# Performance work log

Hardware: AMD Instinct MI355X
Metric: run time of the kernel (lower is better)

The kernel has to match this reference:

```python
import jax, jax.numpy as jnp
import numpy as np
import math

B, S_MAX, D = 16, 4096, 4096
H, H_KV, D_H = 32, 8, 128
REP = H // H_KV
START_POS = S_MAX - 1  # decode at last slot -> attend over full cache


def _rope(t, cos, sin):
    # t: [B, 1, h, D_H]; cos/sin: [1, D_H//2] (per-position rotary factors)
    b, s, h, dh = t.shape
    tr = t.reshape(b, s, h, dh // 2, 2)
    e, o = tr[..., 0], tr[..., 1]          # even / odd components
    c = cos[None, :, None, :]              # [1, 1, 1, D_H//2]
    sn = sin[None, :, None, :]
    out = jnp.stack([e * c - o * sn, e * sn + o * c], axis=-1)
    return out.reshape(b, s, h, dh)


def setup_inputs() -> dict:
    key = jax.random.key(0)
    ks = jax.random.split(key, 8)
    x = jax.random.normal(ks[0], (B, 1, D), dtype=jnp.float32)
    cache_k = jax.random.normal(ks[1], (B, S_MAX, H_KV, D_H), dtype=jnp.float32) * 0.02
    cache_v = jax.random.normal(ks[2], (B, S_MAX, H_KV, D_H), dtype=jnp.float32) * 0.02
    wq = jax.random.normal(ks[3], (D, H * D_H), dtype=jnp.float32) * 0.02
    wk = jax.random.normal(ks[4], (D, H_KV * D_H), dtype=jnp.float32) * 0.02
    wv = jax.random.normal(ks[5], (D, H_KV * D_H), dtype=jnp.float32) * 0.02
    wo = jax.random.normal(ks[6], (H * D_H, D), dtype=jnp.float32) * 0.02
    # real RoPE angles for position START_POS
    inv_freq = 1.0 / (10000.0 ** (np.arange(0, D_H, 2, dtype=np.float32) / D_H))
    ang = np.float32(START_POS) * inv_freq  # [D_H//2]
    freqs_cos = jnp.asarray(np.cos(ang))[None, :]  # [1, 64]
    freqs_sin = jnp.asarray(np.sin(ang))[None, :]
    return {"x": x, "cache_k": cache_k, "cache_v": cache_v,
            "wq": wq, "wk": wk, "wv": wv, "wo": wo,
            "freqs_cos": freqs_cos, "freqs_sin": freqs_sin,
            "start_pos": START_POS}


def reference(x, cache_k, cache_v, wq, wk, wv, wo, freqs_cos, freqs_sin, start_pos):
    b = x.shape[0]
    xq = (x @ wq).reshape(b, 1, H, D_H)
    xk = (x @ wk).reshape(b, 1, H_KV, D_H)
    xv = (x @ wv).reshape(b, 1, H_KV, D_H)
    xq = _rope(xq, freqs_cos, freqs_sin)
    xk = _rope(xk, freqs_cos, freqs_sin)
    # KV-cache append (start_pos is a Python int -> static slice)
    cache_k = jax.lax.dynamic_update_slice(cache_k, xk, (0, start_pos, 0, 0))
    cache_v = jax.lax.dynamic_update_slice(cache_v, xv, (0, start_pos, 0, 0))
    L = start_pos + 1
    keys = cache_k[:, :L]    # [B, L, H_KV, D_H]
    # NOTE: original has `values = repeat_kv(keys, num_rep)` -- values == keys (bug),
    # reproduced faithfully here. cache_v is still written, matching the original.
    q = xq.reshape(b, 1, H_KV, REP, D_H)
    # GQA scores without materializing the repeated KV tensor
    scores = jnp.einsum('bqkrd,bskd->bkrqs', q, keys) / math.sqrt(D_H)
    attn = jax.nn.softmax(scores, axis=-1)
    out = jnp.einsum('bkrqs,bskd->bqkrd', attn, keys)  # values == keys (faithful bug)
    out = out.reshape(b, 1, H * D_H) @ wo
    return out
```

## Files before the change

kernel.cpp:

```cpp
#include <hip/hip_runtime.h>
#include <math.h>

#define BATCH 16
#define SMAX 4096
#define DMODEL 4096
#define NH 32
#define NKV 8
#define NREP 4
#define DH 128
#define QKCOLS 5120
#define NCHUNK 8
#define CHUNK 512
#define TILE 64

__global__ __launch_bounds__(256) void gemv_part(
    const float* __restrict__ in,
    const float* __restrict__ w1, int c1,
    const float* __restrict__ w2, int c2,
    float* __restrict__ part)
{
    const int tile = blockIdx.x;
    const int ch = blockIdx.y;
    const int t = threadIdx.x;
    const int col = tile * 256 + t;
    const int totC = c1 + c2;
    const int d0 = ch * 256;

    __shared__ float xs[BATCH * 256];
    for (int b = 0; b < BATCH; ++b)
        xs[b * 256 + t] = in[(size_t)b * DMODEL + d0 + t];
    __syncthreads();

    const float* w; int stride, wcol;
    if (col < c1) { w = w1; stride = c1; wcol = col; }
    else          { w = w2; stride = c2; wcol = col - c1; }

    float acc[BATCH];
#pragma unroll
    for (int b = 0; b < BATCH; ++b) acc[b] = 0.f;

    const float* wp = w + (size_t)d0 * stride + wcol;
    for (int d = 0; d < 256; d += 4) {
        float wa = wp[(size_t)(d + 0) * stride];
        float wb = wp[(size_t)(d + 1) * stride];
        float wc = wp[(size_t)(d + 2) * stride];
        float wd = wp[(size_t)(d + 3) * stride];
#pragma unroll
        for (int b = 0; b < BATCH; ++b) {
            const float4 xv = *(const float4*)&xs[b * 256 + d];
            float a = acc[b];
            a = fmaf(xv.x, wa, a);
            a = fmaf(xv.y, wb, a);
            a = fmaf(xv.z, wc, a);
            a = fmaf(xv.w, wd, a);
            acc[b] = a;
        }
    }
#pragma unroll
    for (int b = 0; b < BATCH; ++b)
        part[((size_t)ch * BATCH + b) * totC + col] = acc[b];
}

__global__ __launch_bounds__(256) void rope_reduce(
    const float* __restrict__ part,
    const float* __restrict__ fcos, const float* __restrict__ fsin,
    float* __restrict__ xqk)
{
    int g = blockIdx.x * 256 + threadIdx.x;
    int b = g / 2560;
    int po = g % 2560;
    float e = 0.f, o = 0.f;
    const float* p = part + (size_t)b * QKCOLS + 2 * po;
#pragma unroll
    for (int ch = 0; ch < 16; ++ch) {
        float2 v = *(const float2*)(p + (size_t)ch * BATCH * QKCOLS);
        e += v.x; o += v.y;
    }
    int i = po & 63;
    float c = fcos[i], s = fsin[i];
    xqk[(size_t)b * QKCOLS + 2 * po]     = e * c - o * s;
    xqk[(size_t)b * QKCOLS + 2 * po + 1] = e * s + o * c;
}

__global__ __launch_bounds__(256) void attn_part_kernel(
    const float* __restrict__ cache_k,
    const float* __restrict__ xqk,
    const int* __restrict__ sp,
    float* __restrict__ out)
{
    const int chunk = blockIdx.x;
    const int kv = blockIdx.y;
    const int b = blockIdx.z;
    const int t = threadIdx.x;
    const int dl = t & 63;
    const int r = t >> 6;
    const int start_pos = sp[0];

    __shared__ float k_lds[TILE * DH];

    const int h = kv * NREP + r;
    const float* qp = xqk + (size_t)b * QKCOLS + h * DH;
    const int half = dl & 31;
    const int hi = dl >> 5;
    float4 q4 = *(const float4*)(qp + half * 4);
    const float scale = 0.08838834764831845f;
    q4.x *= scale; q4.y *= scale; q4.z *= scale; q4.w *= scale;
    const int row_owned = (half << 1) + hi;

    const float* xknew = xqk + (size_t)b * QKCOLS + DMODEL + kv * DH;
    const float* kbase = cache_k + ((size_t)b * SMAX * NKV + kv) * DH;

    float m_run = -1e30f, l_run = 0.f;
    float2 acc = make_float2(0.f, 0.f);

    for (int tt = 0; tt < CHUNK / TILE; ++tt) {
        const int s_base = chunk * CHUNK + tt * TILE;
#pragma unroll
        for (int it = 0; it < 8; ++it) {
            int f = it * 256 + t;
            int row = f >> 5;
            int c4 = (f & 31) * 4;
            int s = s_base + row;
            const float* src = (s == start_pos) ? (xknew + c4)
                             : (kbase + (size_t)s * (NKV * DH) + c4);
            *(float4*)&k_lds[row * DH + c4] = *(const float4*)src;
        }
        __syncthreads();

        float score_mine = -1e30f;
        for (int jp = 0; jp < 32; ++jp) {
            int row = 2 * jp + hi;
            const float4 k4 = *(const float4*)&k_lds[row * DH + half * 4];
            float partial = q4.x * k4.x + q4.y * k4.y + q4.z * k4.z + q4.w * k4.w;
#pragma unroll
            for (int m = 1; m < 32; m <<= 1)
                partial += __shfl_xor(partial, m, 64);
            if (half == jp) score_mine = partial;
        }
        if (s_base + row_owned > start_pos) score_mine = -1e30f;

        float m_tile = score_mine;
#pragma unroll
        for (int m = 1; m < 64; m <<= 1)
            m_tile = fmaxf(m_tile, __shfl_xor(m_tile, m, 64));
        float m_new = fmaxf(m_run, m_tile);
        float alpha = __expf(m_run - m_new);
        float p_mine = __expf(score_mine - m_new);
        float psum = p_mine;
#pragma unroll
        for (int m = 1; m < 64; m <<= 1)
            psum += __shfl_xor(psum, m, 64);
        l_run = l_run * alpha + psum;
        acc.x *= alpha; acc.y *= alpha;
        m_run = m_new;

        for (int j = 0; j < 64; ++j) {
            int src_lane = (j >> 1) + ((j & 1) << 5);
            float pj = __shfl(p_mine, src_lane, 64);
            const float2 kj = *(const float2*)&k_lds[j * DH + 2 * dl];
            acc.x = fmaf(pj, kj.x, acc.x);
            acc.y = fmaf(pj, kj.y, acc.y);
        }
        __syncthreads();
    }

    float* rec = out + ((((size_t)b * NKV + kv) * NCHUNK + chunk) * NREP + r) * 130;
    rec[2 * dl] = acc.x;
    rec[2 * dl + 1] = acc.y;
    if (dl == 0) { rec[128] = m_run; rec[129] = l_run; }
}

__global__ __launch_bounds__(128) void attn_combine(
    const float* __restrict__ part, float* __restrict__ attn_out)
{
    const int hq = blockIdx.x;
    const int b = blockIdx.y;
    const int kv = hq >> 2, r = hq & 3;
    const int d = threadIdx.x;
    float m_c[NCHUNK], l_c[NCHUNK];
    float M = -1e30f;
#pragma unroll
    for (int c = 0; c < NCHUNK; ++c) {
        const float* rec = part + ((((size_t)b * NKV + kv) * NCHUNK + c) * NREP + r) * 130;
        m_c[c] = rec[128]; l_c[c] = rec[129];
        M = fmaxf(M, m_c[c]);
    }
    float num = 0.f, den = 0.f;
#pragma unroll
    for (int c = 0; c < NCHUNK; ++c) {
        const float* rec = part + ((((size_t)b * NKV + kv) * NCHUNK + c) * NREP + r) * 130;
        float w = __expf(m_c[c] - M);
        num = fmaf(w, rec[d], num);
        den = fmaf(w, l_c[c], den);
    }
    attn_out[(size_t)b * DMODEL + hq * DH + d] = num / den;
}

__global__ __launch_bounds__(256) void reduce_out(
    const float* __restrict__ part, float* __restrict__ out)
{
    int g = blockIdx.x * 256 + threadIdx.x;
    int b = g >> 12, o = g & 4095;
    float s = 0.f;
#pragma unroll
    for (int ch = 0; ch < 16; ++ch)
        s += part[((size_t)ch * BATCH + b) * DMODEL + o];
    out[g] = s;
}

extern "C" void kernel_launch(void* const* d_in, const int* in_sizes, int n_in,
                              void* d_out, int out_size, void* d_ws, size_t ws_size,
                              hipStream_t stream) {
    const float* x       = (const float*)d_in[0];
    const float* cache_k = (const float*)d_in[1];
    const float* wq      = (const float*)d_in[3];
    const float* wk      = (const float*)d_in[4];
    const float* wo      = (const float*)d_in[6];
    const float* fcos    = (const float*)d_in[7];
    const float* fsin    = (const float*)d_in[8];
    const int*   sp      = (const int*)d_in[9];
    float* out = (float*)d_out;
    float* ws  = (float*)d_ws;

    float* part_qk   = ws;
    float* xqk       = part_qk + 1310720;
    float* attn_part = xqk + 81920;
    float* attn_out  = attn_part + 532480;
    float* part_out  = part_qk;

    gemv_part<<<dim3(QKCOLS / 256, 16), 256, 0, stream>>>(x, wq, 4096, wk, 1024, part_qk);
    rope_reduce<<<160, 256, 0, stream>>>(part_qk, fcos, fsin, xqk);
    attn_part_kernel<<<dim3(NCHUNK, NKV, BATCH), 256, 0, stream>>>(cache_k, xqk, sp, attn_part);
    attn_combine<<<dim3(NH, BATCH), 128, 0, stream>>>(attn_part, attn_out);
    gemv_part<<<dim3(DMODEL / 256, 16), 256, 0, stream>>>(attn_out, wo, 4096, nullptr, 0, part_out);
    reduce_out<<<256, 256, 0, stream>>>(part_out, out);
}
```

Measured before the change: 734.7 us.

## Restructure attention to compute all GQA heads per tile and split GEMV depth finer

```diff
diff --git a/kernel.cpp b/kernel.cpp
--- a/kernel.cpp
+++ b/kernel.cpp
@@ -12,47 +12,52 @@
 #define NCHUNK 8
 #define CHUNK 512
 #define TILE 64
+#define NDCH 32
+#define DCH 128
+#define RECS 132
+
+__global__ __launch_bounds__(256) void transpose_x(
+    const float* __restrict__ x, float* __restrict__ xt)
+{
+    int g = blockIdx.x * 256 + threadIdx.x;
+    int b = g >> 12, d = g & 4095;
+    xt[d * BATCH + b] = x[g];
+}
 
 __global__ __launch_bounds__(256) void gemv_part(
-    const float* __restrict__ in,
+    const float* __restrict__ xt,
     const float* __restrict__ w1, int c1,
     const float* __restrict__ w2, int c2,
     float* __restrict__ part)
 {
-    const int tile = blockIdx.x;
+    const int col = blockIdx.x * 256 + threadIdx.x;
     const int ch = blockIdx.y;
-    const int t = threadIdx.x;
-    const int col = tile * 256 + t;
     const int totC = c1 + c2;
-    const int d0 = ch * 256;
-
-    __shared__ float xs[BATCH * 256];
-    for (int b = 0; b < BATCH; ++b)
-        xs[b * 256 + t] = in[(size_t)b * DMODEL + d0 + t];
-    __syncthreads();
+    const int d0 = ch * DCH;
 
     const float* w; int stride, wcol;
     if (col < c1) { w = w1; stride = c1; wcol = col; }
     else          { w = w2; stride = c2; wcol = col - c1; }
 
+    const float* wp = w + (size_t)d0 * stride + wcol;
+    const float* xp = xt + d0 * BATCH;
+
     float acc[BATCH];
 #pragma unroll
     for (int b = 0; b < BATCH; ++b) acc[b] = 0.f;
 
-    const float* wp = w + (size_t)d0 * stride + wcol;
-    for (int d = 0; d < 256; d += 4) {
+    for (int d = 0; d < DCH; d += 4) {
         float wa = wp[(size_t)(d + 0) * stride];
         float wb = wp[(size_t)(d + 1) * stride];
         float wc = wp[(size_t)(d + 2) * stride];
         float wd = wp[(size_t)(d + 3) * stride];
 #pragma unroll
         for (int b = 0; b < BATCH; ++b) {
-            const float4 xv = *(const float4*)&xs[b * 256 + d];
             float a = acc[b];
-            a = fmaf(xv.x, wa, a);
-            a = fmaf(xv.y, wb, a);
-            a = fmaf(xv.z, wc, a);
-            a = fmaf(xv.w, wd, a);
+            a = fmaf(xp[(d + 0) * BATCH + b], wa, a);
+            a = fmaf(xp[(d + 1) * BATCH + b], wb, a);
+            a = fmaf(xp[(d + 2) * BATCH + b], wc, a);
+            a = fmaf(xp[(d + 3) * BATCH + b], wd, a);
             acc[b] = a;
         }
     }
@@ -72,7 +77,7 @@
     float e = 0.f, o = 0.f;
     const float* p = part + (size_t)b * QKCOLS + 2 * po;
 #pragma unroll
-    for (int ch = 0; ch < 16; ++ch) {
+    for (int ch = 0; ch < NDCH; ++ch) {
         float2 v = *(const float2*)(p + (size_t)ch * BATCH * QKCOLS);
         e += v.x; o += v.y;
     }
@@ -86,92 +91,151 @@
     const float* __restrict__ cache_k,
     const float* __restrict__ xqk,
     const int* __restrict__ sp,
-    float* __restrict__ out)
+    float* __restrict__ outp)
 {
     const int chunk = blockIdx.x;
     const int kv = blockIdx.y;
     const int b = blockIdx.z;
     const int t = threadIdx.x;
-    const int dl = t & 63;
-    const int r = t >> 6;
+    const int lane = t & 63;
+    const int w = t >> 6;
     const int start_pos = sp[0];
 
-    __shared__ float k_lds[TILE * DH];
-
-    const int h = kv * NREP + r;
-    const float* qp = xqk + (size_t)b * QKCOLS + h * DH;
-    const int half = dl & 31;
-    const int hi = dl >> 5;
-    float4 q4 = *(const float4*)(qp + half * 4);
-    const float scale = 0.08838834764831845f;
-    q4.x *= scale; q4.y *= scale; q4.z *= scale; q4.w *= scale;
-    const int row_owned = (half << 1) + hi;
-
+    __shared__ __align__(16) float k_lds[TILE * DH];
+    __shared__ __align__(16) float p_lds[TILE * NREP];
+    __shared__ __align__(16) float alpha_lds[NREP];
+
+    const float* qw = xqk + (size_t)b * QKCOLS + (kv * NREP + w) * DH;
     const float* xknew = xqk + (size_t)b * QKCOLS + DMODEL + kv * DH;
     const float* kbase = cache_k + ((size_t)b * SMAX * NKV + kv) * DH;
-
+    const float scale = 0.08838834764831845f;
+
+    const int jhalf = lane >> 5, cqo = lane & 31;
     float m_run = -1e30f, l_run = 0.f;
-    float2 acc = make_float2(0.f, 0.f);
+    float4 acc[NREP];
+#pragma unroll
+    for (int r = 0; r < NREP; ++r) acc[r] = make_float4(0.f, 0.f, 0.f, 0.f);
+
+    float4 pf[8];
+    {
+        int s_base = chunk * CHUNK;
+#pragma unroll
+        for (int it = 0; it < 8; ++it) {
+            int f = it * 256 + t, row = f >> 5, cq = f & 31;
+            int s = s_base + row;
+            const float* src = (s == start_pos) ? (xknew + 4 * cq)
+                             : (kbase + (size_t)s * (NKV * DH) + 4 * cq);
+            pf[it] = *(const float4*)src;
+        }
+    }
 
     for (int tt = 0; tt < CHUNK / TILE; ++tt) {
         const int s_base = chunk * CHUNK + tt * TILE;
+        __syncthreads();
 #pragma unroll
         for (int it = 0; it < 8; ++it) {
-            int f = it * 256 + t;
-            int row = f >> 5;
-            int c4 = (f & 31) * 4;
-            int s = s_base + row;
-            const float* src = (s == start_pos) ? (xknew + c4)
-                             : (kbase + (size_t)s * (NKV * DH) + c4);
-            *(float4*)&k_lds[row * DH + c4] = *(const float4*)src;
+            int f = it * 256 + t, row = f >> 5, cq = f & 31;
+            *(float4*)&k_lds[row * DH + 4 * (cq ^ (row & 7))] = pf[it];
         }
         __syncthreads();
-
-        float score_mine = -1e30f;
-        for (int jp = 0; jp < 32; ++jp) {
-            int row = 2 * jp + hi;
-            const float4 k4 = *(const float4*)&k_lds[row * DH + half * 4];
-            float partial = q4.x * k4.x + q4.y * k4.y + q4.z * k4.z + q4.w * k4.w;
-#pragma unroll
-            for (int m = 1; m < 32; m <<= 1)
-                partial += __shfl_xor(partial, m, 64);
-            if (half == jp) score_mine = partial;
-        }
-        if (s_base + row_owned > start_pos) score_mine = -1e30f;
-
-        float m_tile = score_mine;
+        if (tt + 1 < CHUNK / TILE) {
+            int nb = s_base + TILE;
+#pragma unroll
+            for (int it = 0; it < 8; ++it) {
+                int f = it * 256 + t, row = f >> 5, cq = f & 31;
+                int s = nb + row;
+                const float* src = (s == start_pos) ? (xknew + 4 * cq)
+                                 : (kbase + (size_t)s * (NKV * DH) + 4 * cq);
+                pf[it] = *(const float4*)src;
+            }
+        }
+
+        float sc = 0.f;
+#pragma unroll
+        for (int cq = 0; cq < 32; ++cq) {
+            const float4 k4 = *(const float4*)&k_lds[lane * DH + 4 * (cq ^ (lane & 7))];
+            sc += qw[4 * cq + 0] * k4.x + qw[4 * cq + 1] * k4.y
+                + qw[4 * cq + 2] * k4.z + qw[4 * cq + 3] * k4.w;
+        }
+        sc *= scale;
+        const bool valid = (s_base + lane) <= start_pos;
+        sc = valid ? sc : -1e30f;
+
+        float m_tile = sc;
 #pragma unroll
         for (int m = 1; m < 64; m <<= 1)
             m_tile = fmaxf(m_tile, __shfl_xor(m_tile, m, 64));
         float m_new = fmaxf(m_run, m_tile);
         float alpha = __expf(m_run - m_new);
-        float p_mine = __expf(score_mine - m_new);
-        float psum = p_mine;
+        float p = valid ? __expf(sc - m_new) : 0.f;
+        float ps = p;
 #pragma unroll
         for (int m = 1; m < 64; m <<= 1)
-            psum += __shfl_xor(psum, m, 64);
-        l_run = l_run * alpha + psum;
-        acc.x *= alpha; acc.y *= alpha;
+            ps += __shfl_xor(ps, m, 64);
+        l_run = l_run * alpha + ps;
         m_run = m_new;
-
-        for (int j = 0; j < 64; ++j) {
-            int src_lane = (j >> 1) + ((j & 1) << 5);
-            float pj = __shfl(p_mine, src_lane, 64);
-            const float2 kj = *(const float2*)&k_lds[j * DH + 2 * dl];
-            acc.x = fmaf(pj, kj.x, acc.x);
-            acc.y = fmaf(pj, kj.y, acc.y);
-        }
+        p_lds[lane * NREP + w] = p;
+        if (lane == 0) alpha_lds[w] = alpha;
         __syncthreads();
-    }
-
-    float* rec = out + ((((size_t)b * NKV + kv) * NCHUNK + chunk) * NREP + r) * 130;
-    rec[2 * dl] = acc.x;
-    rec[2 * dl + 1] = acc.y;
-    if (dl == 0) { rec[128] = m_run; rec[129] = l_run; }
+
+        const float4 a4 = *(const float4*)alpha_lds;
+        float al[NREP] = { a4.x, a4.y, a4.z, a4.w };
+#pragma unroll
+        for (int r = 0; r < NREP; ++r) {
+            acc[r].x *= al[r]; acc[r].y *= al[r];
+            acc[r].z *= al[r]; acc[r].w *= al[r];
+        }
+#pragma unroll
+        for (int jj = 0; jj < 8; ++jj) {
+            const int j = 16 * w + 8 * jhalf + jj;
+            const float4 p4 = *(const float4*)&p_lds[j * NREP];
+            const float4 k4 = *(const float4*)&k_lds[j * DH + 4 * (cqo ^ jj)];
+            acc[0].x = fmaf(p4.x, k4.x, acc[0].x);
+            acc[0].y = fmaf(p4.x, k4.y, acc[0].y);
+            acc[0].z = fmaf(p4.x, k4.z, acc[0].z);
+            acc[0].w = fmaf(p4.x, k4.w, acc[0].w);
+            acc[1].x = fmaf(p4.y, k4.x, acc[1].x);
+            acc[1].y = fmaf(p4.y, k4.y, acc[1].y);
+            acc[1].z = fmaf(p4.y, k4.z, acc[1].z);
+            acc[1].w = fmaf(p4.y, k4.w, acc[1].w);
+            acc[2].x = fmaf(p4.z, k4.x, acc[2].x);
+            acc[2].y = fmaf(p4.z, k4.y, acc[2].y);
+            acc[2].z = fmaf(p4.z, k4.z, acc[2].z);
+            acc[2].w = fmaf(p4.z, k4.w, acc[2].w);
+            acc[3].x = fmaf(p4.w, k4.x, acc[3].x);
+            acc[3].y = fmaf(p4.w, k4.y, acc[3].y);
+            acc[3].z = fmaf(p4.w, k4.z, acc[3].z);
+            acc[3].w = fmaf(p4.w, k4.w, acc[3].w);
+        }
+    }
+
+    __syncthreads();
+    float* dst = &k_lds[t * 16];
+    *(float4*)(dst + 0)  = acc[0];
+    *(float4*)(dst + 4)  = acc[1];
+    *(float4*)(dst + 8)  = acc[2];
+    *(float4*)(dst + 12) = acc[3];
+    __syncthreads();
+    if (t < 128) {
+        const int cq2 = t & 31, rep = t >> 5;
+        float4 sum = make_float4(0.f, 0.f, 0.f, 0.f);
+#pragma unroll
+        for (int src = 0; src < 8; ++src) {
+            int tsrc = (src >> 1) * 64 + (src & 1) * 32 + cq2;
+            const float4 v = *(const float4*)&k_lds[tsrc * 16 + rep * 4];
+            sum.x += v.x; sum.y += v.y; sum.z += v.z; sum.w += v.w;
+        }
+        float* rec = outp + ((((size_t)b * NKV + kv) * NCHUNK + chunk) * NREP + rep) * RECS;
+        *(float4*)&rec[4 * cq2] = sum;
+    }
+    if (lane == 0) {
+        float* rec = outp + ((((size_t)b * NKV + kv) * NCHUNK + chunk) * NREP + w) * RECS;
+        rec[128] = m_run; rec[129] = l_run;
+    }
 }
 
 __global__ __launch_bounds__(128) void attn_combine(
-    const float* __restrict__ part, float* __restrict__ attn_out)
+    const float* __restrict__ part, float* __restrict__ attn_out_t)
 {
     const int hq = blockIdx.x;
     const int b = blockIdx.y;
@@ -181,19 +245,19 @@
     float M = -1e30f;
 #pragma unroll
     for (int c = 0; c < NCHUNK; ++c) {
-        const float* rec = part + ((((size_t)b * NKV + kv) * NCHUNK + c) * NREP + r) * 130;
+        const float* rec = part + ((((size_t)b * NKV + kv) * NCHUNK + c) * NREP + r) * RECS;
         m_c[c] = rec[128]; l_c[c] = rec[129];
         M = fmaxf(M, m_c[c]);
     }
     float num = 0.f, den = 0.f;
 #pragma unroll
     for (int c = 0; c < NCHUNK; ++c) {
-        const float* rec = part + ((((size_t)b * NKV + kv) * NCHUNK + c) * NREP + r) * 130;
-        float w = __expf(m_c[c] - M);
-        num = fmaf(w, rec[d], num);
-        den = fmaf(w, l_c[c], den);
-    }
-    attn_out[(size_t)b * DMODEL + hq * DH + d] = num / den;
+        const float* rec = part + ((((size_t)b * NKV + kv) * NCHUNK + c) * NREP + r) * RECS;
+        float wgt = __expf(m_c[c] - M);
+        num = fmaf(wgt, rec[d], num);
+        den = fmaf(wgt, l_c[c], den);
+    }
+    attn_out_t[(size_t)(hq * DH + d) * BATCH + b] = num / den;
 }
 
 __global__ __launch_bounds__(256) void reduce_out(
@@ -203,7 +267,7 @@
     int b = g >> 12, o = g & 4095;
     float s = 0.f;
 #pragma unroll
-    for (int ch = 0; ch < 16; ++ch)
+    for (int ch = 0; ch < NDCH; ++ch)
         s += part[((size_t)ch * BATCH + b) * DMODEL + o];
     out[g] = s;
 }
@@ -222,16 +286,18 @@
     float* out = (float*)d_out;
     float* ws  = (float*)d_ws;
 
-    float* part_qk   = ws;
-    float* xqk       = part_qk + 1310720;
-    float* attn_part = xqk + 81920;
-    float* attn_out  = attn_part + 532480;
-    float* part_out  = part_qk;
-
-    gemv_part<<<dim3(QKCOLS / 256, 16), 256, 0, stream>>>(x, wq, 4096, wk, 1024, part_qk);
+    float* part_qk    = ws;
+    float* xqk        = part_qk + 2621440;
+    float* xt         = xqk + 81920;
+    float* attn_part  = xt + 65536;
+    float* attn_out_t = attn_part + 540672;
+    float* part_out   = part_qk;
+
+    transpose_x<<<256, 256, 0, stream>>>(x, xt);
+    gemv_part<<<dim3(QKCOLS / 256, NDCH), 256, 0, stream>>>(xt, wq, 4096, wk, 1024, part_qk);
     rope_reduce<<<160, 256, 0, stream>>>(part_qk, fcos, fsin, xqk);
     attn_part_kernel<<<dim3(NCHUNK, NKV, BATCH), 256, 0, stream>>>(cache_k, xqk, sp, attn_part);
-    attn_combine<<<dim3(NH, BATCH), 128, 0, stream>>>(attn_part, attn_out);
-    gemv_part<<<dim3(DMODEL / 256, 16), 256, 0, stream>>>(attn_out, wo, 4096, nullptr, 0, part_out);
+    attn_combine<<<dim3(NH, BATCH), 128, 0, stream>>>(attn_part, attn_out_t);
+    gemv_part<<<dim3(DMODEL / 256, NDCH), 256, 0, stream>>>(attn_out_t, wo, 4096, nullptr, 0, part_out);
     reduce_out<<<256, 256, 0, stream>>>(part_out, out);
 }
```

Result: slower. 763.1 us (+3.9%).
